# Performance work log

Measured on AMD Instinct MI355X. Metric: run time of the kernel, lower is better.

The kernel has to match this reference:

```python
import jax, jax.numpy as jnp
import numpy as np

HEADS = 8
HEAD_DIM = 64
INV_TEMP = HEAD_DIM ** -0.5
LN_EPS = 1e-5  # torch nn.LayerNorm default


def layer_norm(x, g, b):
    mu = jnp.mean(x, axis=-1, keepdims=True)
    var = jnp.var(x, axis=-1, keepdims=True)
    return (x - mu) * jax.lax.rsqrt(var + LN_EPS) * g + b


def setup_inputs() -> dict:
    key = jax.random.key(0)
    ks = jax.random.split(key, 10)
    B, P, N, C = 2, 64, 256, 512
    std = C ** -0.5
    return {
        "q": jax.random.normal(ks[0], (B, P, N, C), jnp.float32),
        "k": jax.random.normal(ks[1], (B, P, N, C), jnp.float32),
        "v": jax.random.normal(ks[2], (B, P, N, C), jnp.float32),
        "mask": jax.random.uniform(ks[3], (B, P, 1, N, N), jnp.float32),
        "pos_scores": jax.random.normal(ks[4], (1, 1, HEADS, N, N), jnp.float32),
        "ln_q_g": jnp.ones((C,), jnp.float32), "ln_q_b": jnp.zeros((C,), jnp.float32),
        "ln_k_g": jnp.ones((C,), jnp.float32), "ln_k_b": jnp.zeros((C,), jnp.float32),
        "ln_v_g": jnp.ones((C,), jnp.float32), "ln_v_b": jnp.zeros((C,), jnp.float32),
        "Wq": jax.random.normal(ks[5], (C, C), jnp.float32) * std,
        "Wk": jax.random.normal(ks[6], (C, C), jnp.float32) * std,
        "Wv": jax.random.normal(ks[7], (C, C), jnp.float32) * std,
        "Wo": jax.random.normal(ks[8], (C, C), jnp.float32) * std,
        "bo": jnp.zeros((C,), jnp.float32),
    }


def reference(q, k, v, mask, pos_scores, ln_q_g, ln_q_b, ln_k_g, ln_k_b,
              ln_v_g, ln_v_b, Wq, Wk, Wv, Wo, bo):
    B, P, N, C = q.shape
    # pre-norm + projections (nn.Linear: y = x @ W^T)
    qh = jnp.einsum('bpnc,ec->bpne', layer_norm(q, ln_q_g, ln_q_b), Wq)
    kh = jnp.einsum('bpnc,ec->bpne', layer_norm(k, ln_k_g, ln_k_b), Wk)
    vh = jnp.einsum('bpnc,ec->bpne', layer_norm(v, ln_v_g, ln_v_b), Wv)
    # split heads: b p n (h d) -> b p h n d
    split = lambda t: t.reshape(B, P, N, HEADS, HEAD_DIM).transpose(0, 1, 3, 2, 4)
    qh, kh, vh = split(qh), split(kh), split(vh)
    # windowed attention with additive pos bias and multiplicative mask
    sim = jnp.einsum('bphid,bphjd->bphij', qh, kh) * INV_TEMP
    sim = mask * (sim + pos_scores)
    attn = jax.nn.softmax(sim, axis=-1)
    out = jnp.einsum('bphij,bphjd->bphid', attn, vh)
    # merge heads: b p h n d -> b p n (h d)
    out = out.transpose(0, 1, 3, 2, 4).reshape(B, P, N, C)
    return jnp.einsum('bpnc,ec->bpne', out, Wo) + bo
```

## Files before the change

kernel.cpp:

```cpp
#include <hip/hip_runtime.h>
#include <hip/hip_fp16.h>

#define BP   128
#define NTOK 256
#define CDIM 512
#define ROWS 32768
#define NH   8
#define DH   64

typedef _Float16 h2_t __attribute__((ext_vector_type(2)));
typedef _Float16 h4_t __attribute__((ext_vector_type(4)));
typedef _Float16 h8_t __attribute__((ext_vector_type(8)));
typedef float    f4_t __attribute__((ext_vector_type(4)));

__device__ __forceinline__ void async16(const void* gptr, void* lptr) {
    __builtin_amdgcn_global_load_lds(
        (const __attribute__((address_space(1))) unsigned int*)gptr,
        (__attribute__((address_space(3))) unsigned int*)lptr, 16, 0, 0);
}

__global__ __launch_bounds__(256) void ln_cast(const float* __restrict__ x,
                                               const float* __restrict__ g,
                                               const float* __restrict__ b,
                                               _Float16* __restrict__ y) {
    const int wave = threadIdx.x >> 6, lane = threadIdx.x & 63;
    const size_t row = (size_t)blockIdx.x * 4 + wave;
    const float4* xr = (const float4*)(x + row * CDIM);
    float4 a0 = xr[2 * lane], a1 = xr[2 * lane + 1];
    float s  = a0.x + a0.y + a0.z + a0.w + a1.x + a1.y + a1.z + a1.w;
    float ss = a0.x * a0.x + a0.y * a0.y + a0.z * a0.z + a0.w * a0.w +
               a1.x * a1.x + a1.y * a1.y + a1.z * a1.z + a1.w * a1.w;
#pragma unroll
    for (int off = 32; off; off >>= 1) {
        s  += __shfl_xor(s, off);
        ss += __shfl_xor(ss, off);
    }
    const float mu = s * (1.f / 512.f);
    const float rs = rsqrtf(ss * (1.f / 512.f) - mu * mu + 1e-5f);
    const float4* gp = (const float4*)g;
    const float4* bpp = (const float4*)b;
    float4 g0 = gp[2 * lane], g1 = gp[2 * lane + 1];
    float4 b0 = bpp[2 * lane], b1 = bpp[2 * lane + 1];
    h8_t o;
    o[0] = (_Float16)((a0.x - mu) * rs * g0.x + b0.x);
    o[1] = (_Float16)((a0.y - mu) * rs * g0.y + b0.y);
    o[2] = (_Float16)((a0.z - mu) * rs * g0.z + b0.z);
    o[3] = (_Float16)((a0.w - mu) * rs * g0.w + b0.w);
    o[4] = (_Float16)((a1.x - mu) * rs * g1.x + b1.x);
    o[5] = (_Float16)((a1.y - mu) * rs * g1.y + b1.y);
    o[6] = (_Float16)((a1.z - mu) * rs * g1.z + b1.z);
    o[7] = (_Float16)((a1.w - mu) * rs * g1.w + b1.w);
    ((h8_t*)(y + row * CDIM))[lane] = o;
}

__global__ __launch_bounds__(256) void cast_w4(const float* __restrict__ w0,
                                               const float* __restrict__ w1,
                                               const float* __restrict__ w2,
                                               const float* __restrict__ w3,
                                               _Float16* __restrict__ o) {
    const float* srcs[4] = {w0, w1, w2, w3};
    const float* w = srcs[blockIdx.y];
    const float scale = (blockIdx.y == 0) ? 0.125f : 1.0f;
    _Float16* dst = o + (size_t)blockIdx.y * (CDIM * CDIM);
    const int idx = blockIdx.x * 256 + threadIdx.x;
    float4 v = ((const float4*)w)[idx];
    h4_t ov = {(_Float16)(v.x * scale), (_Float16)(v.y * scale),
               (_Float16)(v.z * scale), (_Float16)(v.w * scale)};
    ((h4_t*)dst)[idx] = ov;
}

template <int MODE>
__global__ __launch_bounds__(256) void gemm_bt(const _Float16* __restrict__ A,
                                               const _Float16* __restrict__ Bw,
                                               _Float16* __restrict__ Ch,
                                               float* __restrict__ Cf,
                                               const float* __restrict__ bias) {
    constexpr int K = CDIM;
    __shared__ __align__(16) _Float16 As[128 * 64];
    __shared__ __align__(16) _Float16 Bs[128 * 64];
    const int t = threadIdx.x;
    const int wave = t >> 6, lane = t & 63;
    const int wm = wave & 1, wn = wave >> 1;
    const size_t rowBase = (size_t)blockIdx.x * 128;
    const int colBase = blockIdx.y * 128;

    f4_t acc[4][4] = {};

    const int srow = t >> 3;
    const int scol = (t & 7) * 8;
    const _Float16* Ap = A + (rowBase + srow) * K + scol;
    const _Float16* Bp = Bw + ((size_t)colBase + srow) * K + scol;
    char* AsB = (char*)As + wave * 1024;
    char* BsB = (char*)Bs + wave * 1024;

    for (int k0 = 0; k0 < K; k0 += 64) {
#pragma unroll
        for (int c = 0; c < 4; ++c) {
            async16(Ap + (size_t)(32 * c) * K + k0, AsB + c * 4096);
            async16(Bp + (size_t)(32 * c) * K + k0, BsB + c * 4096);
        }
        __syncthreads();
#pragma unroll
        for (int kk = 0; kk < 64; kk += 32) {
            h8_t af[4], bf[4];
#pragma unroll
            for (int i = 0; i < 4; ++i)
                af[i] = *(const h8_t*)(As + (wm * 64 + i * 16 + (lane & 15)) * 64 +
                                       kk + (lane >> 4) * 8);
#pragma unroll
            for (int j = 0; j < 4; ++j)
                bf[j] = *(const h8_t*)(Bs + (wn * 64 + j * 16 + (lane & 15)) * 64 +
                                       kk + (lane >> 4) * 8);
#pragma unroll
            for (int i = 0; i < 4; ++i)
#pragma unroll
                for (int j = 0; j < 4; ++j)
                    acc[i][j] = __builtin_amdgcn_mfma_f32_16x16x32_f16(
                        af[i], bf[j], acc[i][j], 0, 0, 0);
        }
        __syncthreads();
    }
#pragma unroll
    for (int i = 0; i < 4; ++i) {
        const size_t growb = rowBase + wm * 64 + i * 16 + ((lane >> 4) * 4);
#pragma unroll
        for (int j = 0; j < 4; ++j) {
            const int gcol = colBase + wn * 64 + j * 16 + (lane & 15);
            if (MODE == 2) {
                const int bp = (int)(growb >> 8), tok = (int)(growb & 255);
                const int hh = gcol >> 6, dd = gcol & 63;
                h4_t w = {(_Float16)acc[i][j][0], (_Float16)acc[i][j][1],
                          (_Float16)acc[i][j][2], (_Float16)acc[i][j][3]};
                *(h4_t*)(Ch + ((size_t)(bp * NH + hh) * DH + dd) * NTOK + tok) = w;
            } else {
#pragma unroll
                for (int r = 0; r < 4; ++r) {
                    const size_t idx = (growb + r) * CDIM + gcol;
                    if (MODE == 0)
                        Ch[idx] = (_Float16)acc[i][j][r];
                    else
                        Cf[idx] = acc[i][j][r] + bias[gcol];
                }
            }
        }
    }
}

__global__ __launch_bounds__(256, 2) void attn_mfma(const _Float16* __restrict__ Q,
                                                    const _Float16* __restrict__ K,
                                                    const _Float16* __restrict__ VT,
                                                    const float* __restrict__ mask,
                                                    const float* __restrict__ pos,
                                                    _Float16* __restrict__ O) {
    const int bp = blockIdx.x, h = blockIdx.y;
    const int t = threadIdx.x;
    const int wave = t >> 6, lane = t & 63;
    const int g = lane >> 4, li = lane & 15;

    __shared__ __align__(16) _Float16 Ks[64 * 72];
    __shared__ __align__(16) _Float16 VTs[64 * 72];
    __shared__ __align__(16) _Float16 Ps[4 * 64 * 72];
    _Float16* Psw = Ps + wave * (64 * 72);

    h8_t qf[4][2];
#pragma unroll
    for (int it = 0; it < 4; ++it)
#pragma unroll
        for (int x = 0; x < 2; ++x)
            qf[it][x] = *(const h8_t*)(Q +
                (size_t)(bp * NTOK + wave * 64 + it * 16 + li) * CDIM +
                h * DH + x * 32 + g * 8);

    const _Float16* Kg = K + ((size_t)(bp * NTOK) + (t >> 2)) * CDIM + h * DH +
                         (t & 3) * 16;
    const _Float16* Vg = VT + ((size_t)(bp * NH + h) * DH + (t >> 2)) * NTOK +
                         (t & 3) * 16;
    const int sOff = (t >> 2) * 72 + (t & 3) * 16;

    h8_t kpre[2], vpre[2];
#pragma unroll
    for (int x = 0; x < 2; ++x) {
        kpre[x] = *(const h8_t*)(Kg + x * 8);
        vpre[x] = *(const h8_t*)(Vg + x * 8);
    }

    f4_t o[4][4] = {};
    float lp[4] = {0.f, 0.f, 0.f, 0.f};

    for (int c = 0; c < 4; ++c) {
#pragma unroll
        for (int x = 0; x < 2; ++x) {
            *(h8_t*)(Ks + sOff + x * 8) = kpre[x];
            *(h8_t*)(VTs + sOff + x * 8) = vpre[x];
        }
        __syncthreads();
        if (c < 3) {
#pragma unroll
            for (int x = 0; x < 2; ++x) {
                kpre[x] = *(const h8_t*)(Kg + (c + 1) * 64 * CDIM + x * 8);
                vpre[x] = *(const h8_t*)(Vg + (c + 1) * 64 + x * 8);
            }
        }
        f4_t s[4][4] = {};
#pragma unroll
        for (int x = 0; x < 2; ++x) {
            h8_t kf[4];
#pragma unroll
            for (int jt = 0; jt < 4; ++jt)
                kf[jt] = *(const h8_t*)(Ks + (jt * 16 + li) * 72 + x * 32 + g * 8);
#pragma unroll
            for (int jt = 0; jt < 4; ++jt)
#pragma unroll
                for (int it = 0; it < 4; ++it)
                    s[jt][it] = __builtin_amdgcn_mfma_f32_16x16x32_f16(
                        kf[jt], qf[it][x], s[jt][it], 0, 0, 0);
        }
#pragma unroll
        for (int it = 0; it < 4; ++it) {
            const int i = wave * 64 + it * 16 + li;
            const size_t base = (size_t)i * NTOK + c * 64 + g * 4;
            const float* mrow = mask + (size_t)bp * (NTOK * NTOK) + base;
            const float* prow = pos + (size_t)h * (NTOK * NTOK) + base;
#pragma unroll
            for (int jt = 0; jt < 4; ++jt) {
                float4 mm = *(const float4*)(mrow + jt * 16);
                float4 pp = *(const float4*)(prow + jt * 16);
                float e0 = __expf((s[jt][it][0] + pp.x) * mm.x);
                float e1 = __expf((s[jt][it][1] + pp.y) * mm.y);
                float e2 = __expf((s[jt][it][2] + pp.z) * mm.z);
                float e3 = __expf((s[jt][it][3] + pp.w) * mm.w);
                lp[it] += (e0 + e1) + (e2 + e3);
                h4_t w = {(_Float16)e0, (_Float16)e1, (_Float16)e2, (_Float16)e3};
                *(h4_t*)(Psw + (it * 16 + li) * 72 + jt * 16 + g * 4) = w;
            }
        }
#pragma unroll
        for (int x = 0; x < 2; ++x) {
            h8_t vf[4], pf[4];
#pragma unroll
            for (int dt = 0; dt < 4; ++dt)
                vf[dt] = *(const h8_t*)(VTs + (dt * 16 + li) * 72 + x * 32 + g * 8);
#pragma unroll
            for (int it = 0; it < 4; ++it)
                pf[it] = *(const h8_t*)(Psw + (it * 16 + li) * 72 + x * 32 + g * 8);
#pragma unroll
            for (int dt = 0; dt < 4; ++dt)
#pragma unroll
                for (int it = 0; it < 4; ++it)
                    o[dt][it] = __builtin_amdgcn_mfma_f32_16x16x32_f16(
                        vf[dt], pf[it], o[dt][it], 0, 0, 0);
        }
        __syncthreads();
    }

    float inv[4];
#pragma unroll
    for (int it = 0; it < 4; ++it) {
        float l = lp[it];
        l += __shfl_xor(l, 16);
        l += __shfl_xor(l, 32);
        inv[it] = __builtin_amdgcn_rcpf(l);
    }
#pragma unroll
    for (int dt = 0; dt < 4; ++dt)
#pragma unroll
        for (int it = 0; it < 4; ++it) {
            const int i = wave * 64 + it * 16 + li;
            h4_t w = {(_Float16)(o[dt][it][0] * inv[it]),
                      (_Float16)(o[dt][it][1] * inv[it]),
                      (_Float16)(o[dt][it][2] * inv[it]),
                      (_Float16)(o[dt][it][3] * inv[it])};
            *(h4_t*)(O + (size_t)(bp * NTOK + i) * CDIM + h * DH + dt * 16 +
                     g * 4) = w;
        }
}

extern "C" void kernel_launch(void* const* d_in, const int* in_sizes, int n_in,
                              void* d_out, int out_size, void* d_ws, size_t ws_size,
                              hipStream_t stream) {
    const float* q    = (const float*)d_in[0];
    const float* k    = (const float*)d_in[1];
    const float* v    = (const float*)d_in[2];
    const float* mask = (const float*)d_in[3];
    const float* pos  = (const float*)d_in[4];
    const float* lnqg = (const float*)d_in[5];
    const float* lnqb = (const float*)d_in[6];
    const float* lnkg = (const float*)d_in[7];
    const float* lnkb = (const float*)d_in[8];
    const float* lnvg = (const float*)d_in[9];
    const float* lnvb = (const float*)d_in[10];
    const float* Wq   = (const float*)d_in[11];
    const float* Wk   = (const float*)d_in[12];
    const float* Wv   = (const float*)d_in[13];
    const float* Wo   = (const float*)d_in[14];
    const float* bo   = (const float*)d_in[15];
    float* out = (float*)d_out;

    char* ws = (char*)d_ws;
    const size_t XSZ = (size_t)ROWS * CDIM * sizeof(_Float16);
    _Float16* XB  = (_Float16*)ws;
    _Float16* WH  = (_Float16*)(ws + XSZ);
    _Float16* QHp = (_Float16*)(ws + XSZ + 4 * (size_t)(CDIM * CDIM) * sizeof(_Float16));
    _Float16* KHp = QHp + (size_t)ROWS * CDIM;
    _Float16* VTg = KHp + (size_t)ROWS * CDIM;

    cast_w4<<<dim3(256, 4), 256, 0, stream>>>(Wq, Wk, Wv, Wo, WH);

    ln_cast<<<8192, 256, 0, stream>>>(q, lnqg, lnqb, XB);
    gemm_bt<0><<<dim3(256, 4), 256, 0, stream>>>(XB, WH + 0 * (CDIM * CDIM), QHp, nullptr, nullptr);
    ln_cast<<<8192, 256, 0, stream>>>(k, lnkg, lnkb, XB);
    gemm_bt<0><<<dim3(256, 4), 256, 0, stream>>>(XB, WH + 1 * (CDIM * CDIM), KHp, nullptr, nullptr);
    ln_cast<<<8192, 256, 0, stream>>>(v, lnvg, lnvb, XB);
    gemm_bt<2><<<dim3(256, 4), 256, 0, stream>>>(XB, WH + 2 * (CDIM * CDIM), VTg, nullptr, nullptr);

    attn_mfma<<<dim3(BP, NH), 256, 0, stream>>>(QHp, KHp, VTg, mask, pos, XB);

    gemm_bt<1><<<dim3(256, 4), 256, 0, stream>>>(XB, WH + 3 * (CDIM * CDIM), nullptr, out, bo);
}
```

Before: 497.0 us.

## Pre-convert mask/pos to fp16 and double-buffer K/V with per-row-block fused attention

Adds a prep kernel that converts the mask and positional bias to fp16 once, halving the bytes the attention kernel reads for them across all heads. The attention kernel double-buffers K/V tiles in LDS so the next chunk's global loads overlap compute with one barrier per chunk. It fuses QK, softmax-exp and PV per 16-row block, which shrinks the per-wave P buffer. It costs an extra conversion pass and extra workspace, and rounding the mask and bias to fp16 adds small error.

```diff
diff --git a/kernel.cpp b/kernel.cpp
--- a/kernel.cpp
+++ b/kernel.cpp
@@ -69,6 +69,26 @@
     ((h4_t*)dst)[idx] = ov;
 }
 
+__global__ __launch_bounds__(256) void prep_hp(const float* __restrict__ mask,
+                                               const float* __restrict__ pos,
+                                               _Float16* __restrict__ maskh,
+                                               _Float16* __restrict__ posh) {
+    const size_t idx = (size_t)blockIdx.x * 256 + threadIdx.x;
+    const float* src;
+    _Float16* dst;
+    size_t j;
+    if (blockIdx.x < 4096) {
+        src = mask; dst = maskh; j = idx;
+    } else {
+        src = pos; dst = posh; j = idx - (size_t)4096 * 256;
+    }
+    float4 a = ((const float4*)src)[2 * j];
+    float4 b = ((const float4*)src)[2 * j + 1];
+    h8_t o = {(_Float16)a.x, (_Float16)a.y, (_Float16)a.z, (_Float16)a.w,
+              (_Float16)b.x, (_Float16)b.y, (_Float16)b.z, (_Float16)b.w};
+    ((h8_t*)dst)[j] = o;
+}
+
 template <int MODE>
 __global__ __launch_bounds__(256) void gemm_bt(const _Float16* __restrict__ A,
                                                const _Float16* __restrict__ Bw,
@@ -146,21 +166,18 @@
     }
 }
 
-__global__ __launch_bounds__(256, 2) void attn_mfma(const _Float16* __restrict__ Q,
-                                                    const _Float16* __restrict__ K,
-                                                    const _Float16* __restrict__ VT,
-                                                    const float* __restrict__ mask,
-                                                    const float* __restrict__ pos,
-                                                    _Float16* __restrict__ O) {
+__global__ __launch_bounds__(256, 2) void attn_mfma2(
+    const _Float16* __restrict__ Q, const _Float16* __restrict__ K,
+    const _Float16* __restrict__ VT, const _Float16* __restrict__ maskh,
+    const _Float16* __restrict__ posh, _Float16* __restrict__ O) {
     const int bp = blockIdx.x, h = blockIdx.y;
     const int t = threadIdx.x;
     const int wave = t >> 6, lane = t & 63;
     const int g = lane >> 4, li = lane & 15;
 
-    __shared__ __align__(16) _Float16 Ks[64 * 72];
-    __shared__ __align__(16) _Float16 VTs[64 * 72];
-    __shared__ __align__(16) _Float16 Ps[4 * 64 * 72];
-    _Float16* Psw = Ps + wave * (64 * 72);
+    __shared__ __align__(16) _Float16 Ks[2][64 * 72];
+    __shared__ __align__(16) _Float16 VTs[2][64 * 72];
+    __shared__ __align__(16) _Float16 Ps[4][16 * 72];
 
     h8_t qf[4][2];
 #pragma unroll
@@ -177,78 +194,91 @@
                          (t & 3) * 16;
     const int sOff = (t >> 2) * 72 + (t & 3) * 16;
 
-    h8_t kpre[2], vpre[2];
-#pragma unroll
-    for (int x = 0; x < 2; ++x) {
-        kpre[x] = *(const h8_t*)(Kg + x * 8);
-        vpre[x] = *(const h8_t*)(Vg + x * 8);
+    {
+        h8_t k0a = *(const h8_t*)(Kg);
+        h8_t k0b = *(const h8_t*)(Kg + 8);
+        h8_t v0a = *(const h8_t*)(Vg);
+        h8_t v0b = *(const h8_t*)(Vg + 8);
+        *(h8_t*)(&Ks[0][sOff]) = k0a;
+        *(h8_t*)(&Ks[0][sOff + 8]) = k0b;
+        *(h8_t*)(&VTs[0][sOff]) = v0a;
+        *(h8_t*)(&VTs[0][sOff + 8]) = v0b;
     }
 
     f4_t o[4][4] = {};
     float lp[4] = {0.f, 0.f, 0.f, 0.f};
-
+    __syncthreads();
+
+#pragma unroll
     for (int c = 0; c < 4; ++c) {
-#pragma unroll
-        for (int x = 0; x < 2; ++x) {
-            *(h8_t*)(Ks + sOff + x * 8) = kpre[x];
-            *(h8_t*)(VTs + sOff + x * 8) = vpre[x];
-        }
-        __syncthreads();
+        const int p = c & 1;
+        h8_t kn0, kn1, vn0, vn1;
         if (c < 3) {
-#pragma unroll
-            for (int x = 0; x < 2; ++x) {
-                kpre[x] = *(const h8_t*)(Kg + (c + 1) * 64 * CDIM + x * 8);
-                vpre[x] = *(const h8_t*)(Vg + (c + 1) * 64 + x * 8);
-            }
-        }
-        f4_t s[4][4] = {};
-#pragma unroll
-        for (int x = 0; x < 2; ++x) {
-            h8_t kf[4];
-#pragma unroll
-            for (int jt = 0; jt < 4; ++jt)
-                kf[jt] = *(const h8_t*)(Ks + (jt * 16 + li) * 72 + x * 32 + g * 8);
-#pragma unroll
-            for (int jt = 0; jt < 4; ++jt)
-#pragma unroll
-                for (int it = 0; it < 4; ++it)
-                    s[jt][it] = __builtin_amdgcn_mfma_f32_16x16x32_f16(
-                        kf[jt], qf[it][x], s[jt][it], 0, 0, 0);
-        }
+            kn0 = *(const h8_t*)(Kg + (size_t)(c + 1) * 64 * CDIM);
+            kn1 = *(const h8_t*)(Kg + (size_t)(c + 1) * 64 * CDIM + 8);
+            vn0 = *(const h8_t*)(Vg + (c + 1) * 64);
+            vn1 = *(const h8_t*)(Vg + (c + 1) * 64 + 8);
+        }
+        h8_t kf[4][2], vf[4][2];
+#pragma unroll
+        for (int jt = 0; jt < 4; ++jt)
+#pragma unroll
+            for (int x = 0; x < 2; ++x)
+                kf[jt][x] = *(const h8_t*)(&Ks[p][(jt * 16 + li) * 72 + x * 32 + g * 8]);
+#pragma unroll
+        for (int dt = 0; dt < 4; ++dt)
+#pragma unroll
+            for (int x = 0; x < 2; ++x)
+                vf[dt][x] = *(const h8_t*)(&VTs[p][(dt * 16 + li) * 72 + x * 32 + g * 8]);
+
 #pragma unroll
         for (int it = 0; it < 4; ++it) {
             const int i = wave * 64 + it * 16 + li;
-            const size_t base = (size_t)i * NTOK + c * 64 + g * 4;
-            const float* mrow = mask + (size_t)bp * (NTOK * NTOK) + base;
-            const float* prow = pos + (size_t)h * (NTOK * NTOK) + base;
+            const _Float16* mrow = maskh + (size_t)bp * (NTOK * NTOK) +
+                                   (size_t)i * NTOK + c * 64 + g * 4;
+            const _Float16* prow = posh + (size_t)h * (NTOK * NTOK) +
+                                   (size_t)i * NTOK + c * 64 + g * 4;
+            h4_t mm[4], pp[4];
 #pragma unroll
             for (int jt = 0; jt < 4; ++jt) {
-                float4 mm = *(const float4*)(mrow + jt * 16);
-                float4 pp = *(const float4*)(prow + jt * 16);
-                float e0 = __expf((s[jt][it][0] + pp.x) * mm.x);
-                float e1 = __expf((s[jt][it][1] + pp.y) * mm.y);
-                float e2 = __expf((s[jt][it][2] + pp.z) * mm.z);
-                float e3 = __expf((s[jt][it][3] + pp.w) * mm.w);
-                lp[it] += (e0 + e1) + (e2 + e3);
+                mm[jt] = *(const h4_t*)(mrow + jt * 16);
+                pp[jt] = *(const h4_t*)(prow + jt * 16);
+            }
+            f4_t s[4] = {};
+#pragma unroll
+            for (int x = 0; x < 2; ++x)
+#pragma unroll
+                for (int jt = 0; jt < 4; ++jt)
+                    s[jt] = __builtin_amdgcn_mfma_f32_16x16x32_f16(
+                        kf[jt][x], qf[it][x], s[jt], 0, 0, 0);
+            float lacc = 0.f;
+#pragma unroll
+            for (int jt = 0; jt < 4; ++jt) {
+                float e0 = __expf((s[jt][0] + (float)pp[jt][0]) * (float)mm[jt][0]);
+                float e1 = __expf((s[jt][1] + (float)pp[jt][1]) * (float)mm[jt][1]);
+                float e2 = __expf((s[jt][2] + (float)pp[jt][2]) * (float)mm[jt][2]);
+                float e3 = __expf((s[jt][3] + (float)pp[jt][3]) * (float)mm[jt][3]);
+                lacc += (e0 + e1) + (e2 + e3);
                 h4_t w = {(_Float16)e0, (_Float16)e1, (_Float16)e2, (_Float16)e3};
-                *(h4_t*)(Psw + (it * 16 + li) * 72 + jt * 16 + g * 4) = w;
+                *(h4_t*)(&Ps[wave][li * 72 + jt * 16 + g * 4]) = w;
             }
-        }
-#pragma unroll
-        for (int x = 0; x < 2; ++x) {
-            h8_t vf[4], pf[4];
+            lp[it] += lacc;
+            h8_t pf0 = *(const h8_t*)(&Ps[wave][li * 72 + g * 8]);
+            h8_t pf1 = *(const h8_t*)(&Ps[wave][li * 72 + 32 + g * 8]);
 #pragma unroll
             for (int dt = 0; dt < 4; ++dt)
-                vf[dt] = *(const h8_t*)(VTs + (dt * 16 + li) * 72 + x * 32 + g * 8);
-#pragma unroll
-            for (int it = 0; it < 4; ++it)
-                pf[it] = *(const h8_t*)(Psw + (it * 16 + li) * 72 + x * 32 + g * 8);
+                o[dt][it] = __builtin_amdgcn_mfma_f32_16x16x32_f16(
+                    vf[dt][0], pf0, o[dt][it], 0, 0, 0);
 #pragma unroll
             for (int dt = 0; dt < 4; ++dt)
-#pragma unroll
-                for (int it = 0; it < 4; ++it)
-                    o[dt][it] = __builtin_amdgcn_mfma_f32_16x16x32_f16(
-                        vf[dt], pf[it], o[dt][it], 0, 0, 0);
+                o[dt][it] = __builtin_amdgcn_mfma_f32_16x16x32_f16(
+                    vf[dt][1], pf1, o[dt][it], 0, 0, 0);
+        }
+        if (c < 3) {
+            *(h8_t*)(&Ks[1 - p][sOff]) = kn0;
+            *(h8_t*)(&Ks[1 - p][sOff + 8]) = kn1;
+            *(h8_t*)(&VTs[1 - p][sOff]) = vn0;
+            *(h8_t*)(&VTs[1 - p][sOff + 8]) = vn1;
         }
         __syncthreads();
     }
@@ -298,13 +328,16 @@
 
     char* ws = (char*)d_ws;
     const size_t XSZ = (size_t)ROWS * CDIM * sizeof(_Float16);
-    _Float16* XB  = (_Float16*)ws;
-    _Float16* WH  = (_Float16*)(ws + XSZ);
-    _Float16* QHp = (_Float16*)(ws + XSZ + 4 * (size_t)(CDIM * CDIM) * sizeof(_Float16));
-    _Float16* KHp = QHp + (size_t)ROWS * CDIM;
-    _Float16* VTg = KHp + (size_t)ROWS * CDIM;
+    _Float16* XB    = (_Float16*)ws;
+    _Float16* WH    = (_Float16*)(ws + XSZ);
+    _Float16* QHp   = (_Float16*)(ws + XSZ + 4 * (size_t)(CDIM * CDIM) * sizeof(_Float16));
+    _Float16* KHp   = QHp + (size_t)ROWS * CDIM;
+    _Float16* VTg   = KHp + (size_t)ROWS * CDIM;
+    _Float16* maskh = VTg + (size_t)ROWS * CDIM;
+    _Float16* posh  = maskh + (size_t)BP * NTOK * NTOK;
 
     cast_w4<<<dim3(256, 4), 256, 0, stream>>>(Wq, Wk, Wv, Wo, WH);
+    prep_hp<<<4352, 256, 0, stream>>>(mask, pos, maskh, posh);
 
     ln_cast<<<8192, 256, 0, stream>>>(q, lnqg, lnqb, XB);
     gemm_bt<0><<<dim3(256, 4), 256, 0, stream>>>(XB, WH + 0 * (CDIM * CDIM), QHp, nullptr, nullptr);
@@ -313,7 +346,7 @@
     ln_cast<<<8192, 256, 0, stream>>>(v, lnvg, lnvb, XB);
     gemm_bt<2><<<dim3(256, 4), 256, 0, stream>>>(XB, WH + 2 * (CDIM * CDIM), VTg, nullptr, nullptr);
 
-    attn_mfma<<<dim3(BP, NH), 256, 0, stream>>>(QHp, KHp, VTg, mask, pos, XB);
+    attn_mfma2<<<dim3(BP, NH), 256, 0, stream>>>(QHp, KHp, VTg, maskh, posh, XB);
 
     gemm_bt<1><<<dim3(256, 4), 256, 0, stream>>>(XB, WH + 3 * (CDIM * CDIM), nullptr, out, bo);
 }
```

Result: slower. 548.0 us (+10.3%).

## Restructure attention kernel per 16-row tile to cut registers and LDS for occupancy

Applied to the files above, without the earlier changes.

The attention kernel now handles one 16-row query tile at a time within each 64-key chunk: QK^T, exp and the PV MFMA run back to back. This shrinks the score accumulators and the per-wave P buffer from 64 rows to 16. Launch bounds rise from 2 to 4 blocks per CU to exploit the lower register and LDS use, and the mask/pos loads are issued before the MFMAs to hide latency. In exchange there are more LDS round-trips for P, K and V fragments are re-read for every tile, and there are extra barriers around the K/V staging.

```diff
diff --git a/kernel.cpp b/kernel.cpp
--- a/kernel.cpp
+++ b/kernel.cpp
@@ -8,7 +8,6 @@
 #define NH   8
 #define DH   64
 
-typedef _Float16 h2_t __attribute__((ext_vector_type(2)));
 typedef _Float16 h4_t __attribute__((ext_vector_type(4)));
 typedef _Float16 h8_t __attribute__((ext_vector_type(8)));
 typedef float    f4_t __attribute__((ext_vector_type(4)));
@@ -146,12 +145,10 @@
     }
 }
 
-__global__ __launch_bounds__(256, 2) void attn_mfma(const _Float16* __restrict__ Q,
-                                                    const _Float16* __restrict__ K,
-                                                    const _Float16* __restrict__ VT,
-                                                    const float* __restrict__ mask,
-                                                    const float* __restrict__ pos,
-                                                    _Float16* __restrict__ O) {
+__global__ __launch_bounds__(256, 4) void attn_mfma3(
+    const _Float16* __restrict__ Q, const _Float16* __restrict__ K,
+    const _Float16* __restrict__ VT, const float* __restrict__ mask,
+    const float* __restrict__ pos, _Float16* __restrict__ O) {
     const int bp = blockIdx.x, h = blockIdx.y;
     const int t = threadIdx.x;
     const int wave = t >> 6, lane = t & 63;
@@ -159,8 +156,7 @@
 
     __shared__ __align__(16) _Float16 Ks[64 * 72];
     __shared__ __align__(16) _Float16 VTs[64 * 72];
-    __shared__ __align__(16) _Float16 Ps[4 * 64 * 72];
-    _Float16* Psw = Ps + wave * (64 * 72);
+    __shared__ __align__(16) _Float16 Ps[4][16 * 72];
 
     h8_t qf[4][2];
 #pragma unroll
@@ -177,80 +173,86 @@
                          (t & 3) * 16;
     const int sOff = (t >> 2) * 72 + (t & 3) * 16;
 
-    h8_t kpre[2], vpre[2];
-#pragma unroll
-    for (int x = 0; x < 2; ++x) {
-        kpre[x] = *(const h8_t*)(Kg + x * 8);
-        vpre[x] = *(const h8_t*)(Vg + x * 8);
-    }
+    h8_t kn0 = *(const h8_t*)(Kg);
+    h8_t kn1 = *(const h8_t*)(Kg + 8);
+    h8_t vn0 = *(const h8_t*)(Vg);
+    h8_t vn1 = *(const h8_t*)(Vg + 8);
+    *(h8_t*)(&Ks[sOff]) = kn0;
+    *(h8_t*)(&Ks[sOff + 8]) = kn1;
+    *(h8_t*)(&VTs[sOff]) = vn0;
+    *(h8_t*)(&VTs[sOff + 8]) = vn1;
 
     f4_t o[4][4] = {};
     float lp[4] = {0.f, 0.f, 0.f, 0.f};
-
+    __syncthreads();
+
+#pragma unroll
     for (int c = 0; c < 4; ++c) {
-#pragma unroll
-        for (int x = 0; x < 2; ++x) {
-            *(h8_t*)(Ks + sOff + x * 8) = kpre[x];
-            *(h8_t*)(VTs + sOff + x * 8) = vpre[x];
-        }
-        __syncthreads();
         if (c < 3) {
-#pragma unroll
-            for (int x = 0; x < 2; ++x) {
-                kpre[x] = *(const h8_t*)(Kg + (c + 1) * 64 * CDIM + x * 8);
-                vpre[x] = *(const h8_t*)(Vg + (c + 1) * 64 + x * 8);
-            }
-        }
-        f4_t s[4][4] = {};
-#pragma unroll
-        for (int x = 0; x < 2; ++x) {
-            h8_t kf[4];
-#pragma unroll
-            for (int jt = 0; jt < 4; ++jt)
-                kf[jt] = *(const h8_t*)(Ks + (jt * 16 + li) * 72 + x * 32 + g * 8);
-#pragma unroll
-            for (int jt = 0; jt < 4; ++jt)
-#pragma unroll
-                for (int it = 0; it < 4; ++it)
-                    s[jt][it] = __builtin_amdgcn_mfma_f32_16x16x32_f16(
-                        kf[jt], qf[it][x], s[jt][it], 0, 0, 0);
+            kn0 = *(const h8_t*)(Kg + (size_t)(c + 1) * 64 * CDIM);
+            kn1 = *(const h8_t*)(Kg + (size_t)(c + 1) * 64 * CDIM + 8);
+            vn0 = *(const h8_t*)(Vg + (c + 1) * 64);
+            vn1 = *(const h8_t*)(Vg + (c + 1) * 64 + 8);
         }
 #pragma unroll
         for (int it = 0; it < 4; ++it) {
             const int i = wave * 64 + it * 16 + li;
-            const size_t base = (size_t)i * NTOK + c * 64 + g * 4;
-            const float* mrow = mask + (size_t)bp * (NTOK * NTOK) + base;
-            const float* prow = pos + (size_t)h * (NTOK * NTOK) + base;
+            const float* mrow = mask + (size_t)bp * (NTOK * NTOK) +
+                                (size_t)i * NTOK + c * 64 + g * 4;
+            const float* prow = pos + (size_t)h * (NTOK * NTOK) +
+                                (size_t)i * NTOK + c * 64 + g * 4;
+            float4 mm[4], pp[4];
 #pragma unroll
             for (int jt = 0; jt < 4; ++jt) {
-                float4 mm = *(const float4*)(mrow + jt * 16);
-                float4 pp = *(const float4*)(prow + jt * 16);
-                float e0 = __expf((s[jt][it][0] + pp.x) * mm.x);
-                float e1 = __expf((s[jt][it][1] + pp.y) * mm.y);
-                float e2 = __expf((s[jt][it][2] + pp.z) * mm.z);
-                float e3 = __expf((s[jt][it][3] + pp.w) * mm.w);
-                lp[it] += (e0 + e1) + (e2 + e3);
+                mm[jt] = *(const float4*)(mrow + jt * 16);
+                pp[jt] = *(const float4*)(prow + jt * 16);
+            }
+            f4_t s[4] = {};
+#pragma unroll
+            for (int x = 0; x < 2; ++x) {
+                h8_t kf[4];
+#pragma unroll
+                for (int jt = 0; jt < 4; ++jt)
+                    kf[jt] = *(const h8_t*)(&Ks[(jt * 16 + li) * 72 + x * 32 + g * 8]);
+#pragma unroll
+                for (int jt = 0; jt < 4; ++jt)
+                    s[jt] = __builtin_amdgcn_mfma_f32_16x16x32_f16(
+                        kf[jt], qf[it][x], s[jt], 0, 0, 0);
+            }
+            float lacc = 0.f;
+#pragma unroll
+            for (int jt = 0; jt < 4; ++jt) {
+                float e0 = __expf((s[jt][0] + pp[jt].x) * mm[jt].x);
+                float e1 = __expf((s[jt][1] + pp[jt].y) * mm[jt].y);
+                float e2 = __expf((s[jt][2] + pp[jt].z) * mm[jt].z);
+                float e3 = __expf((s[jt][3] + pp[jt].w) * mm[jt].w);
+                lacc += (e0 + e1) + (e2 + e3);
                 h4_t w = {(_Float16)e0, (_Float16)e1, (_Float16)e2, (_Float16)e3};
-                *(h4_t*)(Psw + (it * 16 + li) * 72 + jt * 16 + g * 4) = w;
-            }
-        }
-#pragma unroll
-        for (int x = 0; x < 2; ++x) {
-            h8_t vf[4], pf[4];
-#pragma unroll
-            for (int dt = 0; dt < 4; ++dt)
-                vf[dt] = *(const h8_t*)(VTs + (dt * 16 + li) * 72 + x * 32 + g * 8);
-#pragma unroll
-            for (int it = 0; it < 4; ++it)
-                pf[it] = *(const h8_t*)(Psw + (it * 16 + li) * 72 + x * 32 + g * 8);
-#pragma unroll
-            for (int dt = 0; dt < 4; ++dt)
-#pragma unroll
-                for (int it = 0; it < 4; ++it)
+                *(h4_t*)(&Ps[wave][li * 72 + jt * 16 + g * 4]) = w;
+            }
+            lp[it] += lacc;
+            h8_t pf0 = *(const h8_t*)(&Ps[wave][li * 72 + g * 8]);
+            h8_t pf1 = *(const h8_t*)(&Ps[wave][li * 72 + 32 + g * 8]);
+#pragma unroll
+            for (int x = 0; x < 2; ++x) {
+                h8_t vf[4];
+#pragma unroll
+                for (int dt = 0; dt < 4; ++dt)
+                    vf[dt] = *(const h8_t*)(&VTs[(dt * 16 + li) * 72 + x * 32 + g * 8]);
+#pragma unroll
+                for (int dt = 0; dt < 4; ++dt)
                     o[dt][it] = __builtin_amdgcn_mfma_f32_16x16x32_f16(
-                        vf[dt], pf[it], o[dt][it], 0, 0, 0);
-        }
-        __syncthreads();
+                        vf[dt], x ? pf1 : pf0, o[dt][it], 0, 0, 0);
+            }
+        }
+        if (c < 3) {
+            __syncthreads();
+            *(h8_t*)(&Ks[sOff]) = kn0;
+            *(h8_t*)(&Ks[sOff + 8]) = kn1;
+            *(h8_t*)(&VTs[sOff]) = vn0;
+            *(h8_t*)(&VTs[sOff + 8]) = vn1;
+            __syncthreads();
+        }
     }
 
     float inv[4];
@@ -313,7 +315,7 @@
     ln_cast<<<8192, 256, 0, stream>>>(v, lnvg, lnvb, XB);
     gemm_bt<2><<<dim3(256, 4), 256, 0, stream>>>(XB, WH + 2 * (CDIM * CDIM), VTg, nullptr, nullptr);
 
-    attn_mfma<<<dim3(BP, NH), 256, 0, stream>>>(QHp, KHp, VTg, mask, pos, XB);
+    attn_mfma3<<<dim3(BP, NH), 256, 0, stream>>>(QHp, KHp, VTg, mask, pos, XB);
 
     gemm_bt<1><<<dim3(256, 4), 256, 0, stream>>>(XB, WH + 3 * (CDIM * CDIM), nullptr, out, bo);
 }
```

After: 630.8 us. +26.9%, slower.
